# Performance work log

Measured on AMD Instinct MI355X. Metric: run time of the kernel, lower is better.

## Reference

```python
import jax, jax.numpy as jnp
import numpy as np

B, S, D = 128, 512, 768          # batch, seq_len, token_dim
NH, HD = 8, 96                    # num_heads, head_dim = sentence_dim/num_heads
HID = 4 * HD                      # hidden_dim = 384


def setup_inputs() -> dict:
    key = jax.random.key(0)
    ks = jax.random.split(key, 9)
    token_embeddings = jax.random.normal(ks[0], (B, S, D), dtype=jnp.float32)
    # variable-length attention mask (1 for real tokens, 0 for padding)
    lengths = jax.random.randint(ks[1], (B,), S // 2, S + 1)
    attention_mask = (jnp.arange(S)[None, :] < lengths[:, None]).astype(jnp.float32)
    s = 0.02
    P  = jax.random.normal(ks[2], (NH, HD, D),   dtype=jnp.float32) * s
    bP = jnp.zeros((NH, HD), dtype=jnp.float32)
    W1 = jax.random.normal(ks[3], (NH, HID, HD), dtype=jnp.float32) * s
    b1 = jnp.zeros((NH, HID), dtype=jnp.float32)
    W2 = jax.random.normal(ks[4], (NH, HD, HID), dtype=jnp.float32) * s
    b2 = jnp.zeros((NH, HD), dtype=jnp.float32)
    return {"token_embeddings": token_embeddings, "attention_mask": attention_mask,
            "P": P, "bP": bP, "W1": W1, "b1": b1, "W2": W2, "b2": b2}


def reference(token_embeddings, attention_mask, P, bP, W1, b1, W2, b2):
    # per-head projection: H_i = P_i(H)           -> (nh, B, S, HD)
    Hi = jnp.einsum('bsd,ihd->ibsh', token_embeddings, P) + bP[:, None, None, :]
    # scores: W2(relu(W1(H_i)))                   -> (nh, B, S, HD)
    A = jnp.einsum('ibsf,ihf->ibsh',
                   jax.nn.relu(jnp.einsum('ibsh,ifh->ibsf', Hi, W1) + b1[:, None, None, :]),
                   W2) + b2[:, None, None, :]
    # masked softmax over sequence dim (log(mask) adds -inf on padding)
    log_mask = jnp.log(attention_mask)[None, :, :, None]  # (1, B, S, 1)
    A = jax.nn.softmax(A + log_mask, axis=2)
    # weighted sum over tokens                    -> (nh, B, HD)
    v = jnp.sum(Hi * A, axis=2)
    # concat heads: (B, nh*HD) = (B, 768)
    pooled = jnp.transpose(v, (1, 0, 2)).reshape(token_embeddings.shape[0], NH * HD)
    return pooled
```

## Files before the change

### kernel.cpp

```cpp
#include <hip/hip_runtime.h>
#include <stdint.h>


typedef short bf16x8 __attribute__((ext_vector_type(8)));
typedef float f32x4 __attribute__((ext_vector_type(4)));

struct alignas(8) us4 { unsigned short x, y, z, w; };

__device__ __forceinline__ unsigned short f32_to_bf16(float f) {
  union { float f; uint32_t u; } v; v.f = f;
  uint32_t u = v.u;
  uint32_t r = (u + 0x7fffu + ((u >> 16) & 1u)) >> 16;
  return (unsigned short)r;
}

__device__ __forceinline__ float bf16_to_f32(unsigned short h) {
  union { uint32_t u; float f; } v; v.u = ((uint32_t)h) << 16;
  return v.f;
}

__device__ __forceinline__ uint32_t pack_bf16_trunc(float lo, float hi) {
  union { float f; uint32_t u; } a, b; a.f = lo; b.f = hi;
  return __builtin_amdgcn_perm(b.u, a.u, 0x07060302u);
}

__device__ __forceinline__ void g2l16(const unsigned short* g, unsigned short* l) {
  __builtin_amdgcn_global_load_lds((__attribute__((address_space(1))) void*)g,
                                   (__attribute__((address_space(3))) void*)l,
                                   16, 0, 0);
}

__device__ __forceinline__ void stageW(const unsigned short* __restrict__ src,
                                       unsigned short* dst, int w, int lane) {
#pragma unroll
  for (int it = 0; it < 4; ++it)
    g2l16(src + (size_t)((it * 4 + w) * 64 + lane) * 8, &dst[(it * 4 + w) * 512]);
  if (w < 2)
    g2l16(src + (size_t)((16 + w) * 64 + lane) * 8, &dst[(16 + w) * 512]);
}


#define N_X   50331648
#define N_P   589824
#define N_W1  294912
#define N_W2  294912
#define N_HI  50331648


__global__ __launch_bounds__(256) void cast_f32_bf16(
    const float* __restrict__ src, unsigned short* __restrict__ dst, int n4) {
  int idx = blockIdx.x * 256 + threadIdx.x;
  if (idx >= n4) return;
  float4 v = ((const float4*)src)[idx];
  us4 o;
  o.x = f32_to_bf16(v.x);
  o.y = f32_to_bf16(v.y);
  o.z = f32_to_bf16(v.z);
  o.w = f32_to_bf16(v.w);
  ((us4*)dst)[idx] = o;
}


__global__ __launch_bounds__(256) void repack_w1(
    const float* __restrict__ W1, unsigned short* __restrict__ W1bf) {
  const int quarter = blockIdx.x;
  const int hd = quarter >> 2, ph = quarter & 3;
  for (int t = threadIdx.x; t < 1152; t += 256) {
    const int kb = t / 384;
    const int rem = t - kb * 384;
    const int f = rem >> 2, slot = rem & 3;
    const int pos = slot ^ ((f >> 1) & 3);
    const float* src =
        W1 + ((size_t)(hd * 384 + ph * 96 + f)) * 96 + kb * 32 + pos * 8;
    float4 a = *(const float4*)src;
    float4 b = *(const float4*)(src + 4);
    us4 o1 = {f32_to_bf16(a.x), f32_to_bf16(a.y), f32_to_bf16(a.z), f32_to_bf16(a.w)};
    us4 o2 = {f32_to_bf16(b.x), f32_to_bf16(b.y), f32_to_bf16(b.z), f32_to_bf16(b.w)};
    us4* dst = (us4*)(W1bf + (size_t)quarter * 9216 + t * 8);
    dst[0] = o1;
    dst[1] = o2;
  }
}

__global__ __launch_bounds__(256) void repack_w2(
    const float* __restrict__ W2, unsigned short* __restrict__ W2bf) {
  const int quarter = blockIdx.x;
  const int hd = quarter >> 2, ph = quarter & 3;
  for (int t = threadIdx.x; t < 1152; t += 256) {
    const int kb = t / 384;
    const int rem = t - kb * 384;
    const int h = rem >> 2, slot = rem & 3;
    const int pos = slot ^ ((h >> 1) & 3);
    const float* src =
        W2 + ((size_t)(hd * 96 + h)) * 384 + ph * 96 + kb * 32 + pos * 8;
    float4 a = *(const float4*)src;
    float4 b = *(const float4*)(src + 4);
    us4 o1 = {f32_to_bf16(a.x), f32_to_bf16(a.y), f32_to_bf16(a.z), f32_to_bf16(a.w)};
    us4 o2 = {f32_to_bf16(b.x), f32_to_bf16(b.y), f32_to_bf16(b.z), f32_to_bf16(b.w)};
    us4* dst = (us4*)(W2bf + (size_t)quarter * 9216 + t * 8);
    dst[0] = o1;
    dst[1] = o2;
  }
}


__global__ __launch_bounds__(256) void gemm_hi(
    const unsigned short* __restrict__ Xbf,
    const unsigned short* __restrict__ Pbf,
    const float* __restrict__ bP,
    unsigned short* __restrict__ Hi) {
  __shared__ __align__(16) unsigned short As[128 * 32];
  __shared__ __align__(16) unsigned short Bs[128 * 32];

  const int tid = threadIdx.x;
  const int w = tid >> 6;
  const int lane = tid & 63;
  const int r = lane & 15;
  const int q = lane >> 4;

  const int hwid = blockIdx.x;
  const int wkid = (hwid & 7) * 384 + (hwid >> 3);
  const int bn = wkid % 6;
  const int bm = wkid / 6;

  const int wr = w >> 1, wc = w & 1;
  const int psw = q ^ ((r >> 1) & 3);

  f32x4 acc[4][4];
#pragma unroll
  for (int a = 0; a < 4; ++a)
#pragma unroll
    for (int c = 0; c < 4; ++c) acc[a][c] = (f32x4){0.f, 0.f, 0.f, 0.f};

  const int ldr = lane >> 2;
  const int ldc = ((lane & 3) ^ ((lane >> 3) & 3)) * 8;
  const unsigned short* Abase = Xbf + (size_t)(bm * 128) * 768 + ldc;
  const unsigned short* Bbase = Pbf + (size_t)(bn * 128) * 768 + ldc;

  for (int k0 = 0; k0 < 768; k0 += 32) {
    __syncthreads();
    g2l16(Abase + (size_t)(w * 16 + ldr) * 768 + k0, &As[w * 512]);
    g2l16(Abase + (size_t)(64 + w * 16 + ldr) * 768 + k0, &As[(4 + w) * 512]);
    g2l16(Bbase + (size_t)(w * 16 + ldr) * 768 + k0, &Bs[w * 512]);
    g2l16(Bbase + (size_t)(64 + w * 16 + ldr) * 768 + k0, &Bs[(4 + w) * 512]);
    __syncthreads();

    bf16x8 af[4], bfr[4];
#pragma unroll
    for (int t = 0; t < 4; ++t)
      af[t] = *(const bf16x8*)&As[(wr * 64 + t * 16 + r) * 32 + psw * 8];
#pragma unroll
    for (int t = 0; t < 4; ++t)
      bfr[t] = *(const bf16x8*)&Bs[(wc * 64 + t * 16 + r) * 32 + psw * 8];
#pragma unroll
    for (int mt = 0; mt < 4; ++mt)
#pragma unroll
      for (int nt = 0; nt < 4; ++nt)
        acc[mt][nt] = __builtin_amdgcn_mfma_f32_16x16x32_bf16(
            af[mt], bfr[nt], acc[mt][nt], 0, 0, 0);
  }

  const int bb = bm >> 2;
  const int sb = (bm & 3) * 128 + wr * 64;
#pragma unroll
  for (int nt = 0; nt < 4; ++nt) {
    const int n0 = bn * 128 + wc * 64 + nt * 16;
    const int hd = n0 / 96;
    const int hloc = n0 - hd * 96;
    const int kb = hloc >> 5;
    const int col = (hloc & 31) + r;
    const float bias = bP[n0 + r];
    unsigned short* obase =
        Hi + (size_t)(hd * 128 + bb) * 49152 + kb * 16384 + col;
#pragma unroll
    for (int mt = 0; mt < 4; ++mt) {
#pragma unroll
      for (int rg = 0; rg < 4; ++rg) {
        const int s = sb + mt * 16 + q * 4 + rg;
        obase[(size_t)s * 32] = f32_to_bf16(acc[mt][nt][rg] + bias);
      }
    }
  }
}


__global__ __launch_bounds__(256, 2) void mlp_pool(
    const unsigned short* __restrict__ Hi,
    const unsigned short* __restrict__ W1bf,
    const unsigned short* __restrict__ W2bf,
    const float* __restrict__ b1,
    const float* __restrict__ b2,
    const float* __restrict__ mask,
    float* __restrict__ out) {
  __shared__ __align__(16) unsigned short Ws1[3 * 96 * 32];
  __shared__ __align__(16) unsigned short Ws2[3 * 96 * 32];
  __shared__ __align__(16) unsigned short Fs[128 * 104];
  __shared__ __align__(16) float b1s[384];
  __shared__ __align__(16) float b2s[96];
  __shared__ float bias_s[512];
  __shared__ float redA[4][96];
  __shared__ float redB[4][96];

  const int x = blockIdx.x;
  const int b = x & 127;
  const int hd = x >> 7;

  const int tid = threadIdx.x;
  const int w = tid >> 6;
  const int lane = tid & 63;
  const int r = lane & 15;
  const int q = lane >> 4;
  const int psw = q ^ ((r >> 1) & 3);

  if (tid < 96) b2s[tid] = b2[hd * 96 + tid];
  for (int i = tid; i < 384; i += 256) b1s[i] = b1[hd * 384 + i];
  for (int s = tid; s < 512; s += 256)
    bias_s[s] = mask[b * 512 + s] > 0.5f ? 0.f : -1e30f;

  float m_run[6], l_run[6], v_run[6];
#pragma unroll
  for (int nt = 0; nt < 6; ++nt) { m_run[nt] = -3e30f; l_run[nt] = 0.f; v_run[nt] = 0.f; }

  const unsigned short* ysrc = Hi + (size_t)(hd * 128 + b) * 49152;
  const unsigned short* w1h = W1bf + (size_t)(hd * 4) * 9216;
  const unsigned short* w2h = W2bf + (size_t)(hd * 4) * 9216;

  stageW(w1h, Ws1, w, lane);
  __syncthreads();

  for (int c = 0; c < 4; ++c) {
    const unsigned short* yc = ysrc + c * 4096;

    f32x4 acc3[2][6];
#pragma unroll
    for (int sp = 0; sp < 2; ++sp)
#pragma unroll
      for (int nt = 0; nt < 6; ++nt) acc3[sp][nt] = (f32x4){0.f, 0.f, 0.f, 0.f};

    for (int ph = 0; ph < 4; ++ph) {
      bf16x8 bfrg[2][3];
#pragma unroll
      for (int sp = 0; sp < 2; ++sp)
#pragma unroll
        for (int kb = 0; kb < 3; ++kb)
          bfrg[sp][kb] = *(const bf16x8*)(yc + kb * 16384 +
                                          ((w * 2 + sp) * 16 + r) * 32 + q * 8);

      stageW(w2h + ph * 9216, Ws2, w, lane);

      f32x4 acc2[6][2];
#pragma unroll
      for (int ft = 0; ft < 6; ++ft)
#pragma unroll
        for (int sp = 0; sp < 2; ++sp) acc2[ft][sp] = (f32x4){0.f, 0.f, 0.f, 0.f};
#pragma unroll
      for (int kb = 0; kb < 3; ++kb) {
#pragma unroll
        for (int ft = 0; ft < 6; ++ft) {
          bf16x8 afrg = *(const bf16x8*)&Ws1[kb * 3072 + (ft * 16 + r) * 32 + psw * 8];
#pragma unroll
          for (int sp = 0; sp < 2; ++sp)
            acc2[ft][sp] = __builtin_amdgcn_mfma_f32_16x16x32_bf16(
                afrg, bfrg[sp][kb], acc2[ft][sp], 0, 0, 0);
        }
      }
#pragma unroll
      for (int ft = 0; ft < 6; ++ft) {
        float4 bv = *(const float4*)&b1s[ph * 96 + ft * 16 + q * 4];
#pragma unroll
        for (int sp = 0; sp < 2; ++sp) {
          const int s = (w * 2 + sp) * 16 + r;
          float v0 = fmaxf(acc2[ft][sp][0] + bv.x, 0.f);
          float v1 = fmaxf(acc2[ft][sp][1] + bv.y, 0.f);
          float v2 = fmaxf(acc2[ft][sp][2] + bv.z, 0.f);
          float v3 = fmaxf(acc2[ft][sp][3] + bv.w, 0.f);
          uint2 pk;
          pk.x = pack_bf16_trunc(v0, v1);
          pk.y = pack_bf16_trunc(v2, v3);
          *(uint2*)((uint32_t*)&Fs[0] + s * 52 + ft * 8 + q * 2) = pk;
        }
      }
      __syncthreads();

      if (!(c == 3 && ph == 3))
        stageW(w1h + ((ph + 1) & 3) * 9216, Ws1, w, lane);

#pragma unroll
      for (int kb = 0; kb < 3; ++kb) {
        bf16x8 afrg[2];
#pragma unroll
        for (int sp = 0; sp < 2; ++sp)
          afrg[sp] = *(const bf16x8*)&Fs[((w * 2 + sp) * 16 + r) * 104 + kb * 32 + q * 8];
#pragma unroll
        for (int nt = 0; nt < 6; ++nt) {
          bf16x8 bfrg2 = *(const bf16x8*)&Ws2[kb * 3072 + (nt * 16 + r) * 32 + psw * 8];
#pragma unroll
          for (int sp = 0; sp < 2; ++sp)
            acc3[sp][nt] = __builtin_amdgcn_mfma_f32_16x16x32_bf16(
                afrg[sp], bfrg2, acc3[sp][nt], 0, 0, 0);
        }
      }
      __syncthreads();
    }

#pragma unroll
    for (int nt = 0; nt < 6; ++nt) {
      const float b2v = b2s[nt * 16 + r];
      float lm = -3e30f;
#pragma unroll
      for (int sp = 0; sp < 2; ++sp) {
#pragma unroll
        for (int rg = 0; rg < 4; ++rg) {
          const int sl = (w * 2 + sp) * 16 + q * 4 + rg;
          float lg = acc3[sp][nt][rg] + b2v + bias_s[c * 128 + sl];
          lm = fmaxf(lm, lg);
        }
      }
      lm = fmaxf(lm, __shfl_xor(lm, 16));
      lm = fmaxf(lm, __shfl_xor(lm, 32));
      if (q == 0) redA[w][nt * 16 + r] = lm;
    }
    __syncthreads();
#pragma unroll
    for (int nt = 0; nt < 6; ++nt) {
      const int h = nt * 16 + r;
      const unsigned short* yb = yc + (nt >> 1) * 16384 + (nt & 1) * 16 + r;
      const float cm = fmaxf(fmaxf(redA[0][h], redA[1][h]),
                             fmaxf(redA[2][h], redA[3][h]));
      const float mnew = fmaxf(m_run[nt], cm);
      const float sc = __expf(m_run[nt] - mnew);
      m_run[nt] = mnew;
      float lacc = l_run[nt] * sc;
      float vacc = v_run[nt] * sc;
      const float b2v = b2s[h];
#pragma unroll
      for (int sp = 0; sp < 2; ++sp) {
#pragma unroll
        for (int rg = 0; rg < 4; ++rg) {
          const int sl = (w * 2 + sp) * 16 + q * 4 + rg;
          float lg = acc3[sp][nt][rg] + b2v + bias_s[c * 128 + sl];
          float e = __expf(lg - mnew);
          lacc += e;
          vacc += e * bf16_to_f32(yb[(size_t)sl * 32]);
        }
      }
      l_run[nt] = lacc;
      v_run[nt] = vacc;
    }
  }

  __syncthreads();
#pragma unroll
  for (int nt = 0; nt < 6; ++nt) {
    float ls = l_run[nt], vs = v_run[nt];
    ls += __shfl_xor(ls, 16);
    vs += __shfl_xor(vs, 16);
    ls += __shfl_xor(ls, 32);
    vs += __shfl_xor(vs, 32);
    if (q == 0) {
      redA[w][nt * 16 + r] = ls;
      redB[w][nt * 16 + r] = vs;
    }
  }
  __syncthreads();
  if (tid < 96) {
    float ls = redA[0][tid] + redA[1][tid] + redA[2][tid] + redA[3][tid];
    float vs = redB[0][tid] + redB[1][tid] + redB[2][tid] + redB[3][tid];
    out[(size_t)b * 768 + hd * 96 + tid] = vs / ls;
  }
}


extern "C" void kernel_launch(void* const* d_in, const int* in_sizes, int n_in,
                              void* d_out, int out_size, void* d_ws, size_t ws_size,
                              hipStream_t stream) {
  const float* X    = (const float*)d_in[0];
  const float* mask = (const float*)d_in[1];
  const float* P    = (const float*)d_in[2];
  const float* bP   = (const float*)d_in[3];
  const float* W1   = (const float*)d_in[4];
  const float* b1   = (const float*)d_in[5];
  const float* W2   = (const float*)d_in[6];
  const float* b2   = (const float*)d_in[7];
  float* out = (float*)d_out;
  (void)in_sizes; (void)n_in; (void)out_size; (void)ws_size;

  unsigned short* Xbf  = (unsigned short*)d_ws;
  unsigned short* Pbf  = Xbf + N_X;
  unsigned short* W1bf = Pbf + N_P;
  unsigned short* W2bf = W1bf + N_W1;
  unsigned short* Hi   = W2bf + N_W2;

  cast_f32_bf16<<<N_X / 4 / 256, 256, 0, stream>>>(X, Xbf, N_X / 4);
  cast_f32_bf16<<<N_P / 4 / 256, 256, 0, stream>>>(P, Pbf, N_P / 4);
  repack_w1<<<32, 256, 0, stream>>>(W1, W1bf);
  repack_w2<<<32, 256, 0, stream>>>(W2, W2bf);

  gemm_hi<<<3072, 256, 0, stream>>>(Xbf, Pbf, bP, Hi);
  mlp_pool<<<8 * 128, 256, 0, stream>>>(Hi, W1bf, W2bf, b1, b2, mask, out);
}
```

Before: 542.3 us.

## Merge prep kernels and alias W1/F LDS buffers to raise mlp_pool occupancy

```diff
diff --git a/kernel.cpp b/kernel.cpp
--- a/kernel.cpp
+++ b/kernel.cpp
@@ -47,59 +47,59 @@
 #define N_HI  50331648
 
 
-__global__ __launch_bounds__(256) void cast_f32_bf16(
-    const float* __restrict__ src, unsigned short* __restrict__ dst, int n4) {
-  int idx = blockIdx.x * 256 + threadIdx.x;
-  if (idx >= n4) return;
-  float4 v = ((const float4*)src)[idx];
-  us4 o;
-  o.x = f32_to_bf16(v.x);
-  o.y = f32_to_bf16(v.y);
-  o.z = f32_to_bf16(v.z);
-  o.w = f32_to_bf16(v.w);
-  ((us4*)dst)[idx] = o;
-}
-
-
-__global__ __launch_bounds__(256) void repack_w1(
-    const float* __restrict__ W1, unsigned short* __restrict__ W1bf) {
-  const int quarter = blockIdx.x;
-  const int hd = quarter >> 2, ph = quarter & 3;
-  for (int t = threadIdx.x; t < 1152; t += 256) {
-    const int kb = t / 384;
-    const int rem = t - kb * 384;
-    const int f = rem >> 2, slot = rem & 3;
-    const int pos = slot ^ ((f >> 1) & 3);
-    const float* src =
-        W1 + ((size_t)(hd * 384 + ph * 96 + f)) * 96 + kb * 32 + pos * 8;
-    float4 a = *(const float4*)src;
-    float4 b = *(const float4*)(src + 4);
-    us4 o1 = {f32_to_bf16(a.x), f32_to_bf16(a.y), f32_to_bf16(a.z), f32_to_bf16(a.w)};
-    us4 o2 = {f32_to_bf16(b.x), f32_to_bf16(b.y), f32_to_bf16(b.z), f32_to_bf16(b.w)};
-    us4* dst = (us4*)(W1bf + (size_t)quarter * 9216 + t * 8);
-    dst[0] = o1;
-    dst[1] = o2;
-  }
-}
-
-__global__ __launch_bounds__(256) void repack_w2(
-    const float* __restrict__ W2, unsigned short* __restrict__ W2bf) {
-  const int quarter = blockIdx.x;
-  const int hd = quarter >> 2, ph = quarter & 3;
-  for (int t = threadIdx.x; t < 1152; t += 256) {
-    const int kb = t / 384;
-    const int rem = t - kb * 384;
-    const int h = rem >> 2, slot = rem & 3;
-    const int pos = slot ^ ((h >> 1) & 3);
-    const float* src =
-        W2 + ((size_t)(hd * 96 + h)) * 384 + ph * 96 + kb * 32 + pos * 8;
-    float4 a = *(const float4*)src;
-    float4 b = *(const float4*)(src + 4);
-    us4 o1 = {f32_to_bf16(a.x), f32_to_bf16(a.y), f32_to_bf16(a.z), f32_to_bf16(a.w)};
-    us4 o2 = {f32_to_bf16(b.x), f32_to_bf16(b.y), f32_to_bf16(b.z), f32_to_bf16(b.w)};
-    us4* dst = (us4*)(W2bf + (size_t)quarter * 9216 + t * 8);
-    dst[0] = o1;
-    dst[1] = o2;
+__global__ __launch_bounds__(256) void prep(
+    const float* __restrict__ X, const float* __restrict__ P,
+    const float* __restrict__ W1, const float* __restrict__ W2,
+    unsigned short* __restrict__ Xbf, unsigned short* __restrict__ Pbf,
+    unsigned short* __restrict__ W1bf, unsigned short* __restrict__ W2bf) {
+  const int bx = blockIdx.x;
+  const int tid = threadIdx.x;
+  if (bx < 49152) {
+    const int idx = bx * 256 + tid;
+    float4 v = ((const float4*)X)[idx];
+    us4 o = {f32_to_bf16(v.x), f32_to_bf16(v.y), f32_to_bf16(v.z), f32_to_bf16(v.w)};
+    ((us4*)Xbf)[idx] = o;
+  } else if (bx < 49728) {
+    const int idx = (bx - 49152) * 256 + tid;
+    float4 v = ((const float4*)P)[idx];
+    us4 o = {f32_to_bf16(v.x), f32_to_bf16(v.y), f32_to_bf16(v.z), f32_to_bf16(v.w)};
+    ((us4*)Pbf)[idx] = o;
+  } else if (bx < 49760) {
+    const int quarter = bx - 49728;
+    const int hd = quarter >> 2, ph = quarter & 3;
+    for (int t = tid; t < 1152; t += 256) {
+      const int kb = t / 384;
+      const int rem = t - kb * 384;
+      const int f = rem >> 2, slot = rem & 3;
+      const int pos = slot ^ ((f >> 1) & 3);
+      const float* src =
+          W1 + ((size_t)(hd * 384 + ph * 96 + f)) * 96 + kb * 32 + pos * 8;
+      float4 a = *(const float4*)src;
+      float4 b = *(const float4*)(src + 4);
+      us4 o1 = {f32_to_bf16(a.x), f32_to_bf16(a.y), f32_to_bf16(a.z), f32_to_bf16(a.w)};
+      us4 o2 = {f32_to_bf16(b.x), f32_to_bf16(b.y), f32_to_bf16(b.z), f32_to_bf16(b.w)};
+      us4* dst = (us4*)(W1bf + (size_t)quarter * 9216 + t * 8);
+      dst[0] = o1;
+      dst[1] = o2;
+    }
+  } else {
+    const int quarter = bx - 49760;
+    const int hd = quarter >> 2, ph = quarter & 3;
+    for (int t = tid; t < 1152; t += 256) {
+      const int kb = t / 384;
+      const int rem = t - kb * 384;
+      const int h = rem >> 2, slot = rem & 3;
+      const int pos = slot ^ ((h >> 1) & 3);
+      const float* src =
+          W2 + ((size_t)(hd * 96 + h)) * 384 + ph * 96 + kb * 32 + pos * 8;
+      float4 a = *(const float4*)src;
+      float4 b = *(const float4*)(src + 4);
+      us4 o1 = {f32_to_bf16(a.x), f32_to_bf16(a.y), f32_to_bf16(a.z), f32_to_bf16(a.w)};
+      us4 o2 = {f32_to_bf16(b.x), f32_to_bf16(b.y), f32_to_bf16(b.z), f32_to_bf16(b.w)};
+      us4* dst = (us4*)(W2bf + (size_t)quarter * 9216 + t * 8);
+      dst[0] = o1;
+      dst[1] = o2;
+    }
   }
 }
 
@@ -184,7 +184,7 @@
 }
 
 
-__global__ __launch_bounds__(256, 2) void mlp_pool(
+__global__ __launch_bounds__(256, 3) void mlp_pool(
     const unsigned short* __restrict__ Hi,
     const unsigned short* __restrict__ W1bf,
     const unsigned short* __restrict__ W2bf,
@@ -192,9 +192,8 @@
     const float* __restrict__ b2,
     const float* __restrict__ mask,
     float* __restrict__ out) {
-  __shared__ __align__(16) unsigned short Ws1[3 * 96 * 32];
+  __shared__ __align__(16) unsigned short U[128 * 104];
   __shared__ __align__(16) unsigned short Ws2[3 * 96 * 32];
-  __shared__ __align__(16) unsigned short Fs[128 * 104];
   __shared__ __align__(16) float b1s[384];
   __shared__ __align__(16) float b2s[96];
   __shared__ float bias_s[512];
@@ -225,9 +224,6 @@
   const unsigned short* w1h = W1bf + (size_t)(hd * 4) * 9216;
   const unsigned short* w2h = W2bf + (size_t)(hd * 4) * 9216;
 
-  stageW(w1h, Ws1, w, lane);
-  __syncthreads();
-
   for (int c = 0; c < 4; ++c) {
     const unsigned short* yc = ysrc + c * 4096;
 
@@ -238,15 +234,10 @@
       for (int nt = 0; nt < 6; ++nt) acc3[sp][nt] = (f32x4){0.f, 0.f, 0.f, 0.f};
 
     for (int ph = 0; ph < 4; ++ph) {
-      bf16x8 bfrg[2][3];
-#pragma unroll
-      for (int sp = 0; sp < 2; ++sp)
-#pragma unroll
-        for (int kb = 0; kb < 3; ++kb)
-          bfrg[sp][kb] = *(const bf16x8*)(yc + kb * 16384 +
-                                          ((w * 2 + sp) * 16 + r) * 32 + q * 8);
-
+      if (c | ph) __syncthreads();
+      stageW(w1h + ph * 9216, U, w, lane);
       stageW(w2h + ph * 9216, Ws2, w, lane);
+      __syncthreads();
 
       f32x4 acc2[6][2];
 #pragma unroll
@@ -255,15 +246,22 @@
         for (int sp = 0; sp < 2; ++sp) acc2[ft][sp] = (f32x4){0.f, 0.f, 0.f, 0.f};
 #pragma unroll
       for (int kb = 0; kb < 3; ++kb) {
+        bf16x8 bfrg[2];
+#pragma unroll
+        for (int sp = 0; sp < 2; ++sp)
+          bfrg[sp] = *(const bf16x8*)(yc + kb * 16384 +
+                                      ((w * 2 + sp) * 16 + r) * 32 + q * 8);
 #pragma unroll
         for (int ft = 0; ft < 6; ++ft) {
-          bf16x8 afrg = *(const bf16x8*)&Ws1[kb * 3072 + (ft * 16 + r) * 32 + psw * 8];
+          bf16x8 afrg = *(const bf16x8*)&U[kb * 3072 + (ft * 16 + r) * 32 + psw * 8];
 #pragma unroll
           for (int sp = 0; sp < 2; ++sp)
             acc2[ft][sp] = __builtin_amdgcn_mfma_f32_16x16x32_bf16(
-                afrg, bfrg[sp][kb], acc2[ft][sp], 0, 0, 0);
-        }
-      }
+                afrg, bfrg[sp], acc2[ft][sp], 0, 0, 0);
+        }
+      }
+      __syncthreads();
+
 #pragma unroll
       for (int ft = 0; ft < 6; ++ft) {
         float4 bv = *(const float4*)&b1s[ph * 96 + ft * 16 + q * 4];
@@ -277,20 +275,17 @@
           uint2 pk;
           pk.x = pack_bf16_trunc(v0, v1);
           pk.y = pack_bf16_trunc(v2, v3);
-          *(uint2*)((uint32_t*)&Fs[0] + s * 52 + ft * 8 + q * 2) = pk;
+          *(uint2*)((uint32_t*)&U[0] + s * 52 + ft * 8 + q * 2) = pk;
         }
       }
       __syncthreads();
-
-      if (!(c == 3 && ph == 3))
-        stageW(w1h + ((ph + 1) & 3) * 9216, Ws1, w, lane);
 
 #pragma unroll
       for (int kb = 0; kb < 3; ++kb) {
         bf16x8 afrg[2];
 #pragma unroll
         for (int sp = 0; sp < 2; ++sp)
-          afrg[sp] = *(const bf16x8*)&Fs[((w * 2 + sp) * 16 + r) * 104 + kb * 32 + q * 8];
+          afrg[sp] = *(const bf16x8*)&U[((w * 2 + sp) * 16 + r) * 104 + kb * 32 + q * 8];
 #pragma unroll
         for (int nt = 0; nt < 6; ++nt) {
           bf16x8 bfrg2 = *(const bf16x8*)&Ws2[kb * 3072 + (nt * 16 + r) * 32 + psw * 8];
@@ -300,7 +295,6 @@
                 afrg[sp], bfrg2, acc3[sp][nt], 0, 0, 0);
         }
       }
-      __syncthreads();
     }
 
 #pragma unroll
@@ -391,11 +385,7 @@
   unsigned short* W2bf = W1bf + N_W1;
   unsigned short* Hi   = W2bf + N_W2;
 
-  cast_f32_bf16<<<N_X / 4 / 256, 256, 0, stream>>>(X, Xbf, N_X / 4);
-  cast_f32_bf16<<<N_P / 4 / 256, 256, 0, stream>>>(P, Pbf, N_P / 4);
-  repack_w1<<<32, 256, 0, stream>>>(W1, W1bf);
-  repack_w2<<<32, 256, 0, stream>>>(W2, W2bf);
-
+  prep<<<49792, 256, 0, stream>>>(X, P, W1, W2, Xbf, Pbf, W1bf, W2bf);
   gemm_hi<<<3072, 256, 0, stream>>>(Xbf, Pbf, bP, Hi);
   mlp_pool<<<8 * 128, 256, 0, stream>>>(Hi, W1bf, W2bf, b1, b2, mask, out);
 }
```

Measured after the change: 591.6 us. 9.1% more time.
